# Optimization experiments

Hardware: AMD Instinct MI355X
Metric: run time of the kernel (lower is better)

Reference implementation:

```python
import jax, jax.numpy as jnp
import numpy as np

B, N, D = 8, 2048, 1024
DQ, DV = 1024, 1024


def setup_inputs() -> dict:
    key = jax.random.key(0)
    ks = jax.random.split(key, 7)
    s = 1.0 / np.sqrt(D)
    return {
        "x": jax.random.normal(ks[0], (B, N, D), dtype=jnp.float32),
        "Wq": jax.random.uniform(ks[1], (D, DQ), jnp.float32, -s, s),
        "bq": jax.random.uniform(ks[2], (DQ,), jnp.float32, -s, s),
        "Wk": jax.random.uniform(ks[3], (D, DQ), jnp.float32, -s, s),
        "bk": jax.random.uniform(ks[4], (DQ,), jnp.float32, -s, s),
        "Wv": jax.random.uniform(ks[5], (D, DV), jnp.float32, -s, s),
        "bv": jax.random.uniform(ks[6], (DV,), jnp.float32, -s, s),
    }


def reference(x, Wq, bq, Wk, bk, Wv, bv):
    # Linear projections (nn.Linear: x @ W + b)
    Q = jnp.einsum("bnd,dq->bnq", x, Wq) + bq  # [B,N,DQ]
    K = jnp.einsum("bnd,dq->bnq", x, Wk) + bk  # [B,N,DQ]
    V = jnp.einsum("bnd,dv->bnv", x, Wv) + bv  # [B,N,DV]
    # NOTE: original forward does NOT apply the 1/sqrt(dk) scaling.
    scores = jnp.einsum("bnq,bmq->bnm", Q, K)  # [B,N,N]
    attn = jax.nn.softmax(scores, axis=-1)
    out = jnp.einsum("bnm,bmv->bnv", attn, V)  # [B,N,DV]
    return out
```

## Files before the change

### kernel.cpp

```cpp
#include <hip/hip_runtime.h>
#include <hip/hip_bf16.h>
#include <stdint.h>


typedef _Float16 f16;
typedef _Float16 f16x8 __attribute__((ext_vector_type(8)));
typedef _Float16 f16x4 __attribute__((ext_vector_type(4)));
typedef float f32x4 __attribute__((ext_vector_type(4)));

typedef __attribute__((address_space(3))) void lds_void;
typedef const __attribute__((address_space(1))) void gbl_void;

__device__ __forceinline__ void async16(void* l, const void* g) {
    __builtin_amdgcn_global_load_lds(
        reinterpret_cast<gbl_void*>(reinterpret_cast<uintptr_t>(g)),
        reinterpret_cast<lds_void*>(reinterpret_cast<uintptr_t>(l)),
        16, 0, 0);
}

__global__ __launch_bounds__(256) void cast_f32_f16(const float* __restrict__ x,
                                                    f16* __restrict__ y) {
    long i = (long)blockIdx.x * 256 + threadIdx.x;
    float4 v = reinterpret_cast<const float4*>(x)[i];
    f16x4 o = {(f16)v.x, (f16)v.y, (f16)v.z, (f16)v.w};
    reinterpret_cast<f16x4*>(y)[i] = o;
}

__global__ __launch_bounds__(256) void transpose_cast3(const float* __restrict__ W0,
                                                       const float* __restrict__ W1,
                                                       const float* __restrict__ W2,
                                                       f16* __restrict__ wt) {
    const float* W = blockIdx.z == 0 ? W0 : blockIdx.z == 1 ? W1 : W2;
    f16* o = wt + (long)blockIdx.z * 1024 * 1024;
    __shared__ float tile[32][33];
    int c0 = blockIdx.x * 32, r0 = blockIdx.y * 32;
    int tx = threadIdx.x, ty = threadIdx.y;
#pragma unroll
    for (int i = ty; i < 32; i += 8) tile[i][tx] = W[(long)(r0 + i) * 1024 + c0 + tx];
    __syncthreads();
#pragma unroll
    for (int i = ty; i < 32; i += 8) o[(long)(c0 + i) * 1024 + r0 + tx] = (f16)tile[tx][i];
}

template <int MODE>
__global__ __launch_bounds__(512, 2) void gemm256(
    const f16* __restrict__ A, const f16* __restrict__ Bm,
    f16* __restrict__ o16, float* __restrict__ o32,
    const float* __restrict__ bq, const float* __restrict__ bk,
    const float* __restrict__ bv,
    f16* __restrict__ Qo, f16* __restrict__ Ko, f16* __restrict__ Vto) {
    constexpr int LDA = MODE == 2 ? 2048 : 1024;
    constexpr int LDB = MODE == 2 ? 2048 : 1024;
    constexpr int NT = (MODE == 2 ? 2048 : 1024) / 64;

    __shared__ f16 sm[65536];
    char* smb = (char*)sm;

    const int tid = threadIdx.x;
    const int lane = tid & 63;
    const int wv = tid >> 6;
    const int wmi = wv >> 2;
    const int wni = wv & 3;

    const int L = blockIdx.x;
    long mBase, nBase, oOff = 0;
    int nx = 0;
    if (MODE == 0) {
        const int xcd = L & 7, j = L >> 3;
        nx = j >> 3;
        mBase = (long)(xcd * 8 + (j & 7)) * 256;
        nBase = (long)nx * 256;
    } else if (MODE == 1) {
        const int b = L & 7, j = L >> 3;
        mBase = (long)(j & 7) * 256;
        nBase = (long)(j >> 3) * 256;
        A += (long)b * 2048 * 1024;
        Bm += (long)b * 2048 * 1024;
        oOff = (long)b * 2048 * 2048;
    } else {
        const int b = L & 7, j = L >> 3;
        mBase = (long)(j & 7) * 256;
        nBase = (long)(j >> 3) * 256;
        A += (long)b * 2048 * 2048;
        Bm += (long)b * 1024 * 2048;
        oOff = (long)b * 2048 * 1024;
    }

    const int sru = tid >> 3;
    const int sck = (tid & 7) ^ (sru & 7);
    const f16* pA = A + (mBase + sru) * LDA + sck * 8;
    const f16* pB = Bm + (nBase + sru) * LDB + sck * 8;

    auto stA = [&](int bufB, int half, int t) {
        const f16* s = pA + half * 128 * LDA + t * 64;
        char* d = smb + bufB + half * 16384 + tid * 16;
        async16(d, s);
        async16(d + 8192, s + 64 * LDA);
    };
    auto stB = [&](int bufB, int half, int t) {
        const f16* s = pB + half * 128 * LDB + t * 64;
        char* d = smb + bufB + 32768 + half * 16384 + tid * 16;
        async16(d, s);
        async16(d + 8192, s + 64 * LDB);
    };

    const int pc0 = (lane >> 4) ^ (lane & 7);
    const int aBase = (wmi * 128 + (lane & 15)) * 64 + pc0 * 8;
    const int bBase = 16384 + (wni * 64 + (lane & 15)) * 64 + pc0 * 8;

    stA(0, 0, 0); stA(0, 1, 0); stB(0, 0, 0); stB(0, 1, 0);
    stA(65536, 0, 1); stA(65536, 1, 1); stB(65536, 0, 1);
    asm volatile("s_waitcnt vmcnt(6)" ::: "memory");
    __builtin_amdgcn_s_barrier();

    f32x4 acc[8][4] = {};
    for (int t = 0; t < NT; ++t) {
        const int cE = (t & 1) << 15;
        const int cB = (t & 1) << 16;
        const int nB = cB ^ 65536;
        f16x8 a0[8], a1[8], bA[2], bB[2], bC[2], bD[2];
#pragma unroll
        for (int mf = 0; mf < 8; ++mf)
            a0[mf] = *reinterpret_cast<const f16x8*>(&sm[cE + aBase + mf * 1024]);
#pragma unroll
        for (int q = 0; q < 2; ++q)
            bA[q] = *reinterpret_cast<const f16x8*>(&sm[cE + bBase + q * 1024]);
#pragma unroll
        for (int mf = 0; mf < 8; ++mf)
            a1[mf] = *reinterpret_cast<const f16x8*>(&sm[cE + ((aBase + mf * 1024) ^ 32)]);
        if (t + 1 < NT) stB(nB, 1, t + 1);
        __builtin_amdgcn_s_barrier();
        asm volatile("s_waitcnt lgkmcnt(8)" ::: "memory");
#pragma unroll
        for (int mf = 0; mf < 8; ++mf) {
            acc[mf][0] = __builtin_amdgcn_mfma_f32_16x16x32_f16(a0[mf], bA[0], acc[mf][0], 0, 0, 0);
            acc[mf][1] = __builtin_amdgcn_mfma_f32_16x16x32_f16(a0[mf], bA[1], acc[mf][1], 0, 0, 0);
        }
        asm volatile("s_waitcnt lgkmcnt(0)" ::: "memory");
        __builtin_amdgcn_s_barrier();
#pragma unroll
        for (int q = 0; q < 2; ++q)
            bB[q] = *reinterpret_cast<const f16x8*>(&sm[cE + bBase + (2 + q) * 1024]);
        if (t + 2 < NT) stA(cB, 0, t + 2);
        __builtin_amdgcn_s_barrier();
        asm volatile("s_waitcnt lgkmcnt(0)" ::: "memory");
#pragma unroll
        for (int mf = 0; mf < 8; ++mf) {
            acc[mf][2] = __builtin_amdgcn_mfma_f32_16x16x32_f16(a0[mf], bB[0], acc[mf][2], 0, 0, 0);
            acc[mf][3] = __builtin_amdgcn_mfma_f32_16x16x32_f16(a0[mf], bB[1], acc[mf][3], 0, 0, 0);
        }
        __builtin_amdgcn_s_barrier();
#pragma unroll
        for (int q = 0; q < 2; ++q)
            bC[q] = *reinterpret_cast<const f16x8*>(&sm[cE + ((bBase + q * 1024) ^ 32)]);
#pragma unroll
        for (int q = 0; q < 2; ++q)
            bD[q] = *reinterpret_cast<const f16x8*>(&sm[cE + ((bBase + (2 + q) * 1024) ^ 32)]);
        if (t + 2 < NT) stA(cB, 1, t + 2);
        __builtin_amdgcn_s_barrier();
        asm volatile("s_waitcnt lgkmcnt(2)" ::: "memory");
#pragma unroll
        for (int mf = 0; mf < 8; ++mf) {
            acc[mf][0] = __builtin_amdgcn_mfma_f32_16x16x32_f16(a1[mf], bC[0], acc[mf][0], 0, 0, 0);
            acc[mf][1] = __builtin_amdgcn_mfma_f32_16x16x32_f16(a1[mf], bC[1], acc[mf][1], 0, 0, 0);
        }
        asm volatile("s_waitcnt lgkmcnt(0)" ::: "memory");
        __builtin_amdgcn_s_barrier();
        if (t + 2 < NT) stB(cB, 0, t + 2);
        __builtin_amdgcn_s_barrier();
#pragma unroll
        for (int mf = 0; mf < 8; ++mf) {
            acc[mf][2] = __builtin_amdgcn_mfma_f32_16x16x32_f16(a1[mf], bD[0], acc[mf][2], 0, 0, 0);
            acc[mf][3] = __builtin_amdgcn_mfma_f32_16x16x32_f16(a1[mf], bD[1], acc[mf][3], 0, 0, 0);
        }
        if (t < NT - 2) {
            asm volatile("s_waitcnt vmcnt(6)" ::: "memory");
        } else {
            asm volatile("s_waitcnt vmcnt(0)" ::: "memory");
        }
        __builtin_amdgcn_s_barrier();
    }

    const int rq = (lane >> 4) * 4;
    const int cl = lane & 15;
    if (MODE == 0) {
        const int seg = nx >> 2;
        const float* bias = seg == 0 ? bq : seg == 1 ? bk : bv;
        f16* outQK = seg == 0 ? Qo : Ko;
#pragma unroll
        for (int mf = 0; mf < 8; ++mf)
#pragma unroll
            for (int nf = 0; nf < 4; ++nf) {
                const long c = (nBase & 1023) + wni * 64 + nf * 16 + cl;
                const float bb = bias[c];
#pragma unroll
                for (int r = 0; r < 4; ++r) {
                    const long row = mBase + wmi * 128 + mf * 16 + rq + r;
                    const float v = acc[mf][nf][r] + bb;
                    if (seg < 2) {
                        outQK[row * 1024 + c] = (f16)v;
                    } else {
                        Vto[((row >> 11) * 1024 + c) * 2048 + (row & 2047)] = (f16)v;
                    }
                }
            }
    } else if (MODE == 1) {
        f16* o = o16 + oOff;
#pragma unroll
        for (int mf = 0; mf < 8; ++mf)
#pragma unroll
            for (int nf = 0; nf < 4; ++nf) {
                const long col = nBase + wni * 64 + nf * 16 + cl;
#pragma unroll
                for (int r = 0; r < 4; ++r) {
                    const long row = mBase + wmi * 128 + mf * 16 + rq + r;
                    o[row * 2048 + col] = (f16)acc[mf][nf][r];
                }
            }
    } else {
        float* o = o32 + oOff;
#pragma unroll
        for (int mf = 0; mf < 8; ++mf)
#pragma unroll
            for (int nf = 0; nf < 4; ++nf) {
                const long col = nBase + wni * 64 + nf * 16 + cl;
#pragma unroll
                for (int r = 0; r < 4; ++r) {
                    const long row = mBase + wmi * 128 + mf * 16 + rq + r;
                    o[row * 1024 + col] = acc[mf][nf][r];
                }
            }
    }
}

__global__ __launch_bounds__(256) void softmax_rows(const f16* __restrict__ S,
                                                    f16* __restrict__ P) {
    const long row = blockIdx.x;
    const int t = threadIdx.x;
    f16x8 a = reinterpret_cast<const f16x8*>(S + row * 2048)[t];
    float e[8];
    float m = -1e30f;
#pragma unroll
    for (int j = 0; j < 8; ++j) { e[j] = (float)a[j]; m = fmaxf(m, e[j]); }
#pragma unroll
    for (int o = 32; o > 0; o >>= 1) m = fmaxf(m, __shfl_down(m, o, 64));
    __shared__ float red[8];
    if ((t & 63) == 0) red[t >> 6] = m;
    __syncthreads();
    m = fmaxf(fmaxf(red[0], red[1]), fmaxf(red[2], red[3]));
    float s = 0.0f;
#pragma unroll
    for (int j = 0; j < 8; ++j) { e[j] = __expf(e[j] - m); s += e[j]; }
#pragma unroll
    for (int o = 32; o > 0; o >>= 1) s += __shfl_down(s, o, 64);
    if ((t & 63) == 0) red[4 + (t >> 6)] = s;
    __syncthreads();
    s = red[4] + red[5] + red[6] + red[7];
    float inv = 1.0f / s;
    f16x8 o;
#pragma unroll
    for (int j = 0; j < 8; ++j) o[j] = (f16)(e[j] * inv);
    reinterpret_cast<f16x8*>(P + row * 2048)[t] = o;
}

extern "C" void kernel_launch(void* const* d_in, const int* in_sizes, int n_in,
                              void* d_out, int out_size, void* d_ws, size_t ws_size,
                              hipStream_t stream) {
    const float* x  = (const float*)d_in[0];
    const float* Wq = (const float*)d_in[1];
    const float* bq = (const float*)d_in[2];
    const float* Wk = (const float*)d_in[3];
    const float* bk = (const float*)d_in[4];
    const float* Wv = (const float*)d_in[5];
    const float* bv = (const float*)d_in[6];
    float* out = (float*)d_out;
    char* ws = (char*)d_ws;

    f16* Q   = (f16*)(ws + 0);
    f16* Kb  = (f16*)(ws + 33554432);
    f16* Vt  = (f16*)(ws + 67108864);
    f16* S16 = (f16*)(ws + 100663296);
    f16* P   = (f16*)(ws + 167772160);
    f16* xh  = (f16*)(ws + 100663296);
    f16* wt  = (f16*)(ws + 134217728);

    cast_f32_f16<<<16384, 256, 0, stream>>>(x, xh);
    transpose_cast3<<<dim3(32, 32, 3), dim3(32, 8), 0, stream>>>(Wq, Wk, Wv, wt);

    gemm256<0><<<768, 512, 0, stream>>>(xh, wt, nullptr, nullptr,
                                        bq, bk, bv, Q, Kb, Vt);

    gemm256<1><<<512, 512, 0, stream>>>(Q, Kb, S16, nullptr,
                                        nullptr, nullptr, nullptr,
                                        nullptr, nullptr, nullptr);

    softmax_rows<<<16384, 256, 0, stream>>>(S16, P);

    gemm256<2><<<256, 512, 0, stream>>>(P, Vt, nullptr, out,
                                        nullptr, nullptr, nullptr,
                                        nullptr, nullptr, nullptr);
}
```

Before: 399.1 us.

## Use 1024-thread GEMM blocks with 4x4 fragments per wave

Doubles the GEMM workgroup from 512 to 1024 threads (16 waves), so each wave computes a 64x64 sub-tile instead of 128x64 and each thread issues one async LDS load per stage instead of two. The inner-loop schedule is reorganized: A fragments are loaded in two phases, and the next-stage prefetches of A and B are grouped into one point near the end of the iteration. The aim is more waves in flight to hide latency and lower register pressure per thread. The cost is fewer MFMAs per barrier, a single block per CU because the 128 KB LDS is unchanged, and a less interleaved prefetch schedule.

Result: slower. 411.6 us (+3.1%).

```diff
diff --git a/kernel.cpp b/kernel.cpp
--- a/kernel.cpp
+++ b/kernel.cpp
@@ -43,7 +43,7 @@
 }
 
 template <int MODE>
-__global__ __launch_bounds__(512, 2) void gemm256(
+__global__ __launch_bounds__(1024) void gemm256(
     const f16* __restrict__ A, const f16* __restrict__ Bm,
     f16* __restrict__ o16, float* __restrict__ o32,
     const float* __restrict__ bq, const float* __restrict__ bk,
@@ -92,89 +92,80 @@
     const f16* pB = Bm + (nBase + sru) * LDB + sck * 8;
 
     auto stA = [&](int bufB, int half, int t) {
-        const f16* s = pA + half * 128 * LDA + t * 64;
-        char* d = smb + bufB + half * 16384 + tid * 16;
-        async16(d, s);
-        async16(d + 8192, s + 64 * LDA);
+        async16(smb + bufB + half * 16384 + tid * 16,
+                pA + half * 128 * LDA + t * 64);
     };
     auto stB = [&](int bufB, int half, int t) {
-        const f16* s = pB + half * 128 * LDB + t * 64;
-        char* d = smb + bufB + 32768 + half * 16384 + tid * 16;
-        async16(d, s);
-        async16(d + 8192, s + 64 * LDB);
+        async16(smb + bufB + 32768 + half * 16384 + tid * 16,
+                pB + half * 128 * LDB + t * 64);
     };
 
     const int pc0 = (lane >> 4) ^ (lane & 7);
-    const int aBase = (wmi * 128 + (lane & 15)) * 64 + pc0 * 8;
+    const int aBase = (wmi * 64 + (lane & 15)) * 64 + pc0 * 8;
     const int bBase = 16384 + (wni * 64 + (lane & 15)) * 64 + pc0 * 8;
 
     stA(0, 0, 0); stA(0, 1, 0); stB(0, 0, 0); stB(0, 1, 0);
     stA(65536, 0, 1); stA(65536, 1, 1); stB(65536, 0, 1);
-    asm volatile("s_waitcnt vmcnt(6)" ::: "memory");
+    asm volatile("s_waitcnt vmcnt(3)" ::: "memory");
     __builtin_amdgcn_s_barrier();
 
-    f32x4 acc[8][4] = {};
+    f32x4 acc[4][4] = {};
     for (int t = 0; t < NT; ++t) {
         const int cE = (t & 1) << 15;
         const int cB = (t & 1) << 16;
         const int nB = cB ^ 65536;
-        f16x8 a0[8], a1[8], bA[2], bB[2], bC[2], bD[2];
-#pragma unroll
-        for (int mf = 0; mf < 8; ++mf)
-            a0[mf] = *reinterpret_cast<const f16x8*>(&sm[cE + aBase + mf * 1024]);
+        f16x8 ak0[4], ak1[4], bA[2], bB[2], bC[2], bD[2];
+#pragma unroll
+        for (int mf = 0; mf < 4; ++mf)
+            ak0[mf] = *reinterpret_cast<const f16x8*>(&sm[cE + aBase + mf * 1024]);
 #pragma unroll
         for (int q = 0; q < 2; ++q)
             bA[q] = *reinterpret_cast<const f16x8*>(&sm[cE + bBase + q * 1024]);
-#pragma unroll
-        for (int mf = 0; mf < 8; ++mf)
-            a1[mf] = *reinterpret_cast<const f16x8*>(&sm[cE + ((aBase + mf * 1024) ^ 32)]);
         if (t + 1 < NT) stB(nB, 1, t + 1);
         __builtin_amdgcn_s_barrier();
-        asm volatile("s_waitcnt lgkmcnt(8)" ::: "memory");
-#pragma unroll
-        for (int mf = 0; mf < 8; ++mf) {
-            acc[mf][0] = __builtin_amdgcn_mfma_f32_16x16x32_f16(a0[mf], bA[0], acc[mf][0], 0, 0, 0);
-            acc[mf][1] = __builtin_amdgcn_mfma_f32_16x16x32_f16(a0[mf], bA[1], acc[mf][1], 0, 0, 0);
-        }
         asm volatile("s_waitcnt lgkmcnt(0)" ::: "memory");
+#pragma unroll
+        for (int mf = 0; mf < 4; ++mf) {
+            acc[mf][0] = __builtin_amdgcn_mfma_f32_16x16x32_f16(ak0[mf], bA[0], acc[mf][0], 0, 0, 0);
+            acc[mf][1] = __builtin_amdgcn_mfma_f32_16x16x32_f16(ak0[mf], bA[1], acc[mf][1], 0, 0, 0);
+        }
         __builtin_amdgcn_s_barrier();
 #pragma unroll
         for (int q = 0; q < 2; ++q)
             bB[q] = *reinterpret_cast<const f16x8*>(&sm[cE + bBase + (2 + q) * 1024]);
-        if (t + 2 < NT) stA(cB, 0, t + 2);
         __builtin_amdgcn_s_barrier();
         asm volatile("s_waitcnt lgkmcnt(0)" ::: "memory");
 #pragma unroll
-        for (int mf = 0; mf < 8; ++mf) {
-            acc[mf][2] = __builtin_amdgcn_mfma_f32_16x16x32_f16(a0[mf], bB[0], acc[mf][2], 0, 0, 0);
-            acc[mf][3] = __builtin_amdgcn_mfma_f32_16x16x32_f16(a0[mf], bB[1], acc[mf][3], 0, 0, 0);
-        }
-        __builtin_amdgcn_s_barrier();
+        for (int mf = 0; mf < 4; ++mf) {
+            acc[mf][2] = __builtin_amdgcn_mfma_f32_16x16x32_f16(ak0[mf], bB[0], acc[mf][2], 0, 0, 0);
+            acc[mf][3] = __builtin_amdgcn_mfma_f32_16x16x32_f16(ak0[mf], bB[1], acc[mf][3], 0, 0, 0);
+        }
+        __builtin_amdgcn_s_barrier();
+#pragma unroll
+        for (int mf = 0; mf < 4; ++mf)
+            ak1[mf] = *reinterpret_cast<const f16x8*>(&sm[cE + ((aBase + mf * 1024) ^ 32)]);
 #pragma unroll
         for (int q = 0; q < 2; ++q)
             bC[q] = *reinterpret_cast<const f16x8*>(&sm[cE + ((bBase + q * 1024) ^ 32)]);
 #pragma unroll
         for (int q = 0; q < 2; ++q)
             bD[q] = *reinterpret_cast<const f16x8*>(&sm[cE + ((bBase + (2 + q) * 1024) ^ 32)]);
-        if (t + 2 < NT) stA(cB, 1, t + 2);
-        __builtin_amdgcn_s_barrier();
-        asm volatile("s_waitcnt lgkmcnt(2)" ::: "memory");
-#pragma unroll
-        for (int mf = 0; mf < 8; ++mf) {
-            acc[mf][0] = __builtin_amdgcn_mfma_f32_16x16x32_f16(a1[mf], bC[0], acc[mf][0], 0, 0, 0);
-            acc[mf][1] = __builtin_amdgcn_mfma_f32_16x16x32_f16(a1[mf], bC[1], acc[mf][1], 0, 0, 0);
-        }
+        __builtin_amdgcn_s_barrier();
         asm volatile("s_waitcnt lgkmcnt(0)" ::: "memory");
-        __builtin_amdgcn_s_barrier();
-        if (t + 2 < NT) stB(cB, 0, t + 2);
-        __builtin_amdgcn_s_barrier();
-#pragma unroll
-        for (int mf = 0; mf < 8; ++mf) {
-            acc[mf][2] = __builtin_amdgcn_mfma_f32_16x16x32_f16(a1[mf], bD[0], acc[mf][2], 0, 0, 0);
-            acc[mf][3] = __builtin_amdgcn_mfma_f32_16x16x32_f16(a1[mf], bD[1], acc[mf][3], 0, 0, 0);
+#pragma unroll
+        for (int mf = 0; mf < 4; ++mf) {
+            acc[mf][0] = __builtin_amdgcn_mfma_f32_16x16x32_f16(ak1[mf], bC[0], acc[mf][0], 0, 0, 0);
+            acc[mf][1] = __builtin_amdgcn_mfma_f32_16x16x32_f16(ak1[mf], bC[1], acc[mf][1], 0, 0, 0);
+        }
+        __builtin_amdgcn_s_barrier();
+        if (t + 2 < NT) { stA(cB, 0, t + 2); stA(cB, 1, t + 2); stB(cB, 0, t + 2); }
+#pragma unroll
+        for (int mf = 0; mf < 4; ++mf) {
+            acc[mf][2] = __builtin_amdgcn_mfma_f32_16x16x32_f16(ak1[mf], bD[0], acc[mf][2], 0, 0, 0);
+            acc[mf][3] = __builtin_amdgcn_mfma_f32_16x16x32_f16(ak1[mf], bD[1], acc[mf][3], 0, 0, 0);
         }
         if (t < NT - 2) {
-            asm volatile("s_waitcnt vmcnt(6)" ::: "memory");
+            asm volatile("s_waitcnt vmcnt(3)" ::: "memory");
         } else {
             asm volatile("s_waitcnt vmcnt(0)" ::: "memory");
         }
@@ -188,14 +179,14 @@
         const float* bias = seg == 0 ? bq : seg == 1 ? bk : bv;
         f16* outQK = seg == 0 ? Qo : Ko;
 #pragma unroll
-        for (int mf = 0; mf < 8; ++mf)
+        for (int mf = 0; mf < 4; ++mf)
 #pragma unroll
             for (int nf = 0; nf < 4; ++nf) {
                 const long c = (nBase & 1023) + wni * 64 + nf * 16 + cl;
                 const float bb = bias[c];
 #pragma unroll
                 for (int r = 0; r < 4; ++r) {
-                    const long row = mBase + wmi * 128 + mf * 16 + rq + r;
+                    const long row = mBase + wmi * 64 + mf * 16 + rq + r;
                     const float v = acc[mf][nf][r] + bb;
                     if (seg < 2) {
                         outQK[row * 1024 + c] = (f16)v;
@@ -207,26 +198,26 @@
     } else if (MODE == 1) {
         f16* o = o16 + oOff;
 #pragma unroll
-        for (int mf = 0; mf < 8; ++mf)
+        for (int mf = 0; mf < 4; ++mf)
 #pragma unroll
             for (int nf = 0; nf < 4; ++nf) {
                 const long col = nBase + wni * 64 + nf * 16 + cl;
 #pragma unroll
                 for (int r = 0; r < 4; ++r) {
-                    const long row = mBase + wmi * 128 + mf * 16 + rq + r;
+                    const long row = mBase + wmi * 64 + mf * 16 + rq + r;
                     o[row * 2048 + col] = (f16)acc[mf][nf][r];
                 }
             }
     } else {
         float* o = o32 + oOff;
 #pragma unroll
-        for (int mf = 0; mf < 8; ++mf)
+        for (int mf = 0; mf < 4; ++mf)
 #pragma unroll
             for (int nf = 0; nf < 4; ++nf) {
                 const long col = nBase + wni * 64 + nf * 16 + cl;
 #pragma unroll
                 for (int r = 0; r < 4; ++r) {
-                    const long row = mBase + wmi * 128 + mf * 16 + rq + r;
+                    const long row = mBase + wmi * 64 + mf * 16 + rq + r;
                     o[row * 1024 + col] = acc[mf][nf][r];
                 }
             }
@@ -287,16 +278,16 @@
     cast_f32_f16<<<16384, 256, 0, stream>>>(x, xh);
     transpose_cast3<<<dim3(32, 32, 3), dim3(32, 8), 0, stream>>>(Wq, Wk, Wv, wt);
 
-    gemm256<0><<<768, 512, 0, stream>>>(xh, wt, nullptr, nullptr,
-                                        bq, bk, bv, Q, Kb, Vt);
-
-    gemm256<1><<<512, 512, 0, stream>>>(Q, Kb, S16, nullptr,
-                                        nullptr, nullptr, nullptr,
-                                        nullptr, nullptr, nullptr);
+    gemm256<0><<<768, 1024, 0, stream>>>(xh, wt, nullptr, nullptr,
+                                         bq, bk, bv, Q, Kb, Vt);
+
+    gemm256<1><<<512, 1024, 0, stream>>>(Q, Kb, S16, nullptr,
+                                         nullptr, nullptr, nullptr,
+                                         nullptr, nullptr, nullptr);
 
     softmax_rows<<<16384, 256, 0, stream>>>(S16, P);
 
-    gemm256<2><<<256, 512, 0, stream>>>(P, Vt, nullptr, out,
-                                        nullptr, nullptr, nullptr,
-                                        nullptr, nullptr, nullptr);
-}
+    gemm256<2><<<256, 1024, 0, stream>>>(P, Vt, nullptr, out,
+                                         nullptr, nullptr, nullptr,
+                                         nullptr, nullptr, nullptr);
+}
```
